# Kernel tuning notes

Hardware: AMD Instinct MI355X
Metric: run time of the kernel (lower is better)

Reference implementation:

```python
import jax, jax.numpy as jnp
import numpy as np

NUM_NODES = 100000
NUM_REL = 3
IN_C, HID_C, OUT_C = 128, 64, 32
E, P = 1600000, 200000


def setup_inputs() -> dict:
    key = jax.random.key(0)
    ks = jax.random.split(key, 16)
    inp = {
        "x": jax.random.normal(ks[0], (NUM_NODES, IN_C), dtype=jnp.float32),
        "edge_index": jax.random.randint(ks[1], (2, E), 0, NUM_NODES),
        "edge_type": jax.random.randint(ks[2], (E,), 0, NUM_REL),
        "pred_edges": jax.random.randint(ks[3], (2, P), 0, NUM_NODES),
        # RGCN layer 1
        "W1": jax.random.normal(ks[4], (NUM_REL, IN_C, HID_C), dtype=jnp.float32) * 0.05,
        "root1": jax.random.normal(ks[5], (IN_C, HID_C), dtype=jnp.float32) * 0.05,
        "b1": jnp.zeros((HID_C,), dtype=jnp.float32),
        # RGCN layer 2
        "W2": jax.random.normal(ks[6], (NUM_REL, HID_C, OUT_C), dtype=jnp.float32) * 0.05,
        "root2": jax.random.normal(ks[7], (HID_C, OUT_C), dtype=jnp.float32) * 0.05,
        "b2": jnp.zeros((OUT_C,), dtype=jnp.float32),
        # decoder MLP: Linear(2*OUT_C, HID_C) -> ReLU -> Linear(HID_C, 1)
        "Wd1": jax.random.normal(ks[8], (2 * OUT_C, HID_C), dtype=jnp.float32) * 0.05,
        "bd1": jnp.zeros((HID_C,), dtype=jnp.float32),
        "Wd2": jax.random.normal(ks[9], (HID_C, 1), dtype=jnp.float32) * 0.05,
        "bd2": jnp.zeros((1,), dtype=jnp.float32),
    }
    return inp


def rgcn_conv(x, edge_index, edge_type, W, root, b):
    """PyG RGCNConv: per-relation mean aggregation + root transform + bias."""
    src, dst = edge_index[0], edge_index[1]
    n = x.shape[0]
    xs = x[src]  # [E, in] single gather reused across relations
    out = x @ root + b
    for r in range(W.shape[0]):  # small fixed relation count
        mask = (edge_type == r)
        msg = jnp.where(mask[:, None], xs @ W[r], 0.0)  # [E, out]
        summed = jax.ops.segment_sum(msg, dst, num_segments=n)
        cnt = jax.ops.segment_sum(mask.astype(x.dtype), dst, num_segments=n)
        out = out + summed / jnp.maximum(cnt, 1.0)[:, None]
    return out


def reference(x, edge_index, edge_type, pred_edges, W1, root1, b1, W2, root2, b2, Wd1, bd1, Wd2, bd2):
    # encode (eval mode: dropout is identity)
    z = jax.nn.relu(rgcn_conv(x, edge_index, edge_type, W1, root1, b1))
    z = rgcn_conv(z, edge_index, edge_type, W2, root2, b2)
    # decode
    src, dst = pred_edges[0], pred_edges[1]
    ef = jnp.concatenate([z[src], z[dst]], axis=1)  # [P, 2*OUT_C]
    h = jax.nn.relu(ef @ Wd1 + bd1)
    return (h @ Wd2 + bd2).squeeze(-1)  # [P]
```

## Files before the change

kernel.cpp:

```cpp
#include <hip/hip_runtime.h>
#include <hip/hip_bf16.h>


typedef short bf16x8 __attribute__((ext_vector_type(8)));
typedef float f32x4 __attribute__((ext_vector_type(4)));
typedef float f32x2 __attribute__((ext_vector_type(2)));

__device__ __forceinline__ unsigned short f2bf(float f) {
  union { float f; unsigned u; } x; x.f = f;
  unsigned r = x.u + 0x7FFF + ((x.u >> 16) & 1);
  return (unsigned short)(r >> 16);
}
__device__ __forceinline__ float bf2f(unsigned short h) {
  union { unsigned u; float f; } x; x.u = ((unsigned)h) << 16;
  return x.f;
}
__device__ __forceinline__ f32x2 bfpair(unsigned u) {
  union { unsigned u; float f; } a, b;
  a.u = u << 16; b.u = u & 0xFFFF0000u;
  f32x2 r; r[0] = a.f; r[1] = b.f; return r;
}
__device__ __forceinline__ unsigned pk2(float a, float b) {
  return (unsigned)f2bf(a) | ((unsigned)f2bf(b) << 16);
}

template <int K, int TN>
__device__ __forceinline__ void pack_one(
    int e, const float* __restrict__ W, const float* __restrict__ root,
    ushort* __restrict__ Bh, ushort* __restrict__ Bl) {
  int slab = e / (K * TN), r = e % (K * TN);
  int k = r / TN, n = r % TN;
  float v = (slab < 3) ? W[(size_t)slab * K * TN + k * TN + n] : root[(size_t)k * TN + n];
  int kc = k >> 5, quad = (k >> 3) & 3, j = k & 7, nt = n >> 4, nn = n & 15;
  int NTt = TN / 16;
  int didx = slab * K * TN + ((kc * NTt + nt) * 64 + quad * 16 + nn) * 8 + j;
  unsigned short h = f2bf(v);
  Bh[didx] = h;
  Bl[didx] = f2bf(v - bf2f(h));
}

__global__ __launch_bounds__(256) void hist_pack_kernel(
    const int* __restrict__ ei, int* __restrict__ hist, int E, int tile, int NBUCK,
    const float* __restrict__ W1, const float* __restrict__ root1,
    ushort* __restrict__ Bh1, ushort* __restrict__ Bl1,
    const float* __restrict__ W2, const float* __restrict__ root2,
    ushort* __restrict__ Bh2, ushort* __restrict__ Bl2,
    const float* __restrict__ Wd1, ushort* __restrict__ Bd1h) {
  int tid = threadIdx.x;
  if (blockIdx.x >= 256) {
    int e = (blockIdx.x - 256) * 256 + tid;
    if (e < 32768) {
      pack_one<128, 64>(e, W1, root1, Bh1, Bl1);
    } else if (e < 32768 + 8192) {
      pack_one<64, 32>(e - 32768, W2, root2, Bh2, Bl2);
    } else if (e < 32768 + 8192 + 4096) {
      int r = e - 32768 - 8192;
      int k = r >> 6, n = r & 63;
      int kc = k >> 5, quad = (k >> 3) & 3, j = k & 7, nt = n >> 4, nn = n & 15;
      Bd1h[((kc * 4 + nt) * 64 + quad * 16 + nn) * 8 + j] = f2bf(Wd1[k * 64 + n]);
    }
    return;
  }
  __shared__ int lh[512];
  for (int i = tid; i < 512; i += 256) lh[i] = 0;
  __syncthreads();
  int e0 = blockIdx.x * tile, e1 = min(E, e0 + tile);
  for (int e = e0 + tid; e < e1; e += 256) atomicAdd(&lh[ei[E + e] >> 8], 1);
  __syncthreads();
  for (int i = tid; i < NBUCK; i += 256) hist[i * 256 + blockIdx.x] = lh[i];
}

__device__ __forceinline__ void gemm1_body(
    int bid, int4* __restrict__ bsm,
    const float* __restrict__ A, const ushort* __restrict__ Bh,
    const ushort* __restrict__ Bl, const float* __restrict__ bias,
    ushort* __restrict__ Hb, float* __restrict__ z, int n) {
  constexpr int K = 128, TN = 64;
  constexpr int KC = K / 32;
  constexpr int NTt = TN / 16;
  constexpr int HALF = K * TN / 8;
  const int tid = threadIdx.x;
  const int w = tid >> 6, lane = tid & 63;
  const int quad = lane >> 4, nn = lane & 15;
  const int rowBase = bid * 64 + w * 16;

  int row = rowBase + nn;
  if (row >= n) row = n - 1;
  const float* ap = &A[(size_t)row * K + quad * 8];
  bf16x8 ah[KC], al[KC];
#pragma unroll
  for (int kc = 0; kc < KC; kc++) {
    float4 f0 = *(const float4*)(ap + kc * 32);
    float4 f1 = *(const float4*)(ap + kc * 32 + 4);
    float f[8] = {f0.x, f0.y, f0.z, f0.w, f1.x, f1.y, f1.z, f1.w};
#pragma unroll
    for (int j = 0; j < 8; j++) {
      unsigned short h = f2bf(f[j]);
      ah[kc][j] = (short)h;
      al[kc][j] = (short)f2bf(f[j] - bf2f(h));
    }
  }

  const short* bsp = (const short*)bsm;

#pragma unroll 1
  for (int slab = 0; slab < 4; slab++) {
    __syncthreads();
    {
      const int4* gh = (const int4*)(Bh + (size_t)slab * K * TN);
      for (int i = tid; i < HALF; i += 256) bsm[i] = gh[i];
      if (slab == 3) {
        const int4* gl = (const int4*)(Bl + (size_t)slab * K * TN);
        for (int i = tid; i < HALF; i += 256) bsm[HALF + i] = gl[i];
      }
    }
    __syncthreads();

    f32x4 acc[NTt];
#pragma unroll
    for (int j = 0; j < NTt; j++) acc[j] = (f32x4){0.f, 0.f, 0.f, 0.f};

#pragma unroll
    for (int kc = 0; kc < KC; kc++) {
#pragma unroll
      for (int nt = 0; nt < NTt; nt++) {
        bf16x8 b = *(const bf16x8*)&bsp[((kc * NTt + nt) * 64 + lane) * 8];
        acc[nt] = __builtin_amdgcn_mfma_f32_16x16x32_bf16(ah[kc], b, acc[nt], 0, 0, 0);
        acc[nt] = __builtin_amdgcn_mfma_f32_16x16x32_bf16(al[kc], b, acc[nt], 0, 0, 0);
      }
    }
    if (slab == 3) {
#pragma unroll
      for (int kc = 0; kc < KC; kc++) {
#pragma unroll
        for (int nt = 0; nt < NTt; nt++) {
          bf16x8 b = *(const bf16x8*)&bsp[(HALF * 8) + ((kc * NTt + nt) * 64 + lane) * 8];
          acc[nt] = __builtin_amdgcn_mfma_f32_16x16x32_bf16(ah[kc], b, acc[nt], 0, 0, 0);
        }
      }
    }

    int grow0 = rowBase + quad * 4;
#pragma unroll
    for (int nt = 0; nt < NTt; nt++) {
      int col = nt * 16 + nn;
#pragma unroll
      for (int rg = 0; rg < 4; rg++) {
        int grow = grow0 + rg;
        if (grow < n) {
          float v = acc[nt][rg];
          if (slab == 3) z[(size_t)grow * TN + col] = v + bias[col];
          else Hb[((size_t)slab * n + grow) * TN + col] = f2bf(v);
        }
      }
    }
  }
}


__global__ __launch_bounds__(256, 4) void scan_rows_gemm_kernel(
    int* __restrict__ hist, int* __restrict__ rowsum, int nChain, int gemmBase,
    const float* __restrict__ A, const ushort* __restrict__ Bh,
    const ushort* __restrict__ Bl, const float* __restrict__ bias,
    ushort* __restrict__ Hb, float* __restrict__ z, int n) {
  __shared__ int4 smem[2048];
  if ((int)blockIdx.x >= nChain) {
    gemm1_body(gemmBase + (int)blockIdx.x - nChain, smem, A, Bh, Bl, bias, Hb, z, n);
    return;
  }
  int* sA = (int*)smem;
  int* sB = sA + 256;
  int t = threadIdx.x;
  int* row = hist + blockIdx.x * 256;
  int v = row[t];
  sA[t] = v;
  __syncthreads();
  int* src = sA; int* dst = sB;
  for (int off = 1; off < 256; off <<= 1) {
    int x = src[t];
    if (t >= off) x += src[t - off];
    dst[t] = x;
    __syncthreads();
    int* tmp = src; src = dst; dst = tmp;
  }
  row[t] = src[t] - v;
  if (t == 255) rowsum[blockIdx.x] = src[255];
}

__global__ __launch_bounds__(256, 4) void scan_top_gemm_kernel(
    const int* __restrict__ rowsum, int* __restrict__ rowbase, int NBUCK, int E,
    int nChain, int gemmBase,
    const float* __restrict__ A, const ushort* __restrict__ Bh,
    const ushort* __restrict__ Bl, const float* __restrict__ bias,
    ushort* __restrict__ Hb, float* __restrict__ z, int n) {
  __shared__ int4 smem[2048];
  if ((int)blockIdx.x >= nChain) {
    gemm1_body(gemmBase + (int)blockIdx.x - nChain, smem, A, Bh, Bl, bias, Hb, z, n);
    return;
  }
  int* sA = (int*)smem;
  int* sB = sA + 256;
  int t = threadIdx.x;
  int e0 = 2 * t, e1 = 2 * t + 1;
  int v0 = (e0 < NBUCK) ? rowsum[e0] : 0;
  int v1 = (e1 < NBUCK) ? rowsum[e1] : 0;
  int v = v0 + v1;
  sA[t] = v;
  __syncthreads();
  int* src = sA; int* dst = sB;
  for (int off = 1; off < 256; off <<= 1) {
    int x = src[t];
    if (t >= off) x += src[t - off];
    dst[t] = x;
    __syncthreads();
    int* tmp = src; src = dst; dst = tmp;
  }
  int excl = src[t] - v;
  if (e0 < NBUCK) rowbase[e0] = excl;
  if (e1 < NBUCK) rowbase[e1] = excl + v0;
  if (t == 0) rowbase[NBUCK] = E;
}

__global__ __launch_bounds__(256, 4) void part_scatter_gemm_kernel(
    const int* __restrict__ ei, const int* __restrict__ et,
    const int* __restrict__ hist, const int* __restrict__ rowbase,
    unsigned* __restrict__ rec, int E, int tile, int NBUCK,
    int nChain, int gemmBase,
    const float* __restrict__ A, const ushort* __restrict__ Bh,
    const ushort* __restrict__ Bl, const float* __restrict__ bias,
    ushort* __restrict__ Hb, float* __restrict__ z, int n) {
  __shared__ int4 smem[2048];
  if ((int)blockIdx.x >= nChain) {
    gemm1_body(gemmBase + (int)blockIdx.x - nChain, smem, A, Bh, Bl, bias, Hb, z, n);
    return;
  }
  int* ctr = (int*)smem;
  int tid = threadIdx.x;
  for (int i = tid; i < NBUCK; i += 256)
    ctr[i] = hist[i * 256 + blockIdx.x] + rowbase[i];
  __syncthreads();
  int e0 = blockIdx.x * tile, e1 = min(E, e0 + tile);
  for (int e = e0 + tid; e < e1; e += 256) {
    int s = ei[e];
    int d = ei[E + e];
    int t = et[e];
    int p = atomicAdd(&ctr[d >> 8], 1);
    rec[p] = (unsigned)(s | (t << 20) | ((d & 255) << 22));
  }
}

__global__ __launch_bounds__(256, 4) void bucket_build_gemm_kernel(
    const unsigned* __restrict__ rec, const int* __restrict__ rowbase,
    int2* __restrict__ sd, int2* __restrict__ erec, int N,
    int nChain, int gemmBase,
    const float* __restrict__ A, const ushort* __restrict__ Bh,
    const ushort* __restrict__ Bl, const float* __restrict__ bias,
    ushort* __restrict__ Hb, float* __restrict__ z) {
  __shared__ int4 smem[2048];
  if ((int)blockIdx.x >= nChain) {
    gemm1_body(gemmBase + (int)blockIdx.x - nChain, smem, A, Bh, Bl, bias, Hb, z, N);
    return;
  }
  int* c3 = (int*)smem;
  int* sA = c3 + 768;
  int* sB = sA + 256;
  int* cur = sB + 256;
  int tid = threadIdx.x;
  int dstBase = blockIdx.x << 8;
  int bs = rowbase[blockIdx.x], be = rowbase[blockIdx.x + 1];
  for (int i = tid; i < 768; i += 256) c3[i] = 0;
  __syncthreads();
  for (int i = bs + tid; i < be; i += 256) {
    unsigned r = rec[i];
    atomicAdd(&c3[((r >> 20) & 3) * 256 + (r >> 22)], 1);
  }
  __syncthreads();
  int dgv = c3[tid] + c3[256 + tid] + c3[512 + tid];
  sA[tid] = dgv;
  __syncthreads();
  int* src = sA; int* dst = sB;
  for (int off = 1; off < 256; off <<= 1) {
    int x = src[tid];
    if (tid >= off) x += src[tid - off];
    dst[tid] = x;
    __syncthreads();
    int* tmp = src; src = dst; dst = tmp;
  }
  int excl = src[tid] - dgv;
  cur[tid] = bs + excl;
  if (dstBase + tid < N) sd[dstBase + tid] = make_int2(bs + excl, dgv);
  __syncthreads();
  for (int i = bs + tid; i < be; i += 256) {
    unsigned r = rec[i];
    int dloc = r >> 22;
    int t = (r >> 20) & 3;
    int p = atomicAdd(&cur[dloc], 1);
    float sc = 1.0f / (float)max(c3[t * 256 + dloc], 1);
    erec[p] = make_int2(t * N + (int)(r & 0xFFFFF), __float_as_int(sc));
  }
}

__global__ __launch_bounds__(256, 4) void mfma_gemm2_kernel(
    const ushort* __restrict__ Ab, const ushort* __restrict__ Bh,
    const ushort* __restrict__ Bl, const float* __restrict__ bias,
    ushort* __restrict__ Hb, float* __restrict__ z2r, int n) {
  constexpr int KC = 2, NTt = 2, HALF = 64 * 32 / 8;
  __shared__ int4 bsm[2 * HALF];
  const int tid = threadIdx.x;
  const int w = tid >> 6, lane = tid & 63;
  const int quad = lane >> 4, nn = lane & 15;
  const int rowBase = blockIdx.x * 64 + w * 16;

  int row = rowBase + nn;
  if (row >= n) row = n - 1;
  const ushort* ap = &Ab[(size_t)row * 64 + quad * 8];
  bf16x8 ah[KC];
  ah[0] = *(const bf16x8*)(ap);
  ah[1] = *(const bf16x8*)(ap + 32);

  const short* bsp = (const short*)bsm;

#pragma unroll 1
  for (int slab = 0; slab < 4; slab++) {
    __syncthreads();
    {
      const int4* gh = (const int4*)(Bh + (size_t)slab * 64 * 32);
      for (int i = tid; i < HALF; i += 256) bsm[i] = gh[i];
      if (slab == 3) {
        const int4* gl = (const int4*)(Bl + (size_t)slab * 64 * 32);
        for (int i = tid; i < HALF; i += 256) bsm[HALF + i] = gl[i];
      }
    }
    __syncthreads();

    f32x4 acc[NTt];
#pragma unroll
    for (int j = 0; j < NTt; j++) acc[j] = (f32x4){0.f, 0.f, 0.f, 0.f};

#pragma unroll
    for (int kc = 0; kc < KC; kc++) {
#pragma unroll
      for (int nt = 0; nt < NTt; nt++) {
        bf16x8 b = *(const bf16x8*)&bsp[((kc * NTt + nt) * 64 + lane) * 8];
        acc[nt] = __builtin_amdgcn_mfma_f32_16x16x32_bf16(ah[kc], b, acc[nt], 0, 0, 0);
      }
    }
    if (slab == 3) {
#pragma unroll
      for (int kc = 0; kc < KC; kc++) {
#pragma unroll
        for (int nt = 0; nt < NTt; nt++) {
          bf16x8 b = *(const bf16x8*)&bsp[(HALF * 8) + ((kc * NTt + nt) * 64 + lane) * 8];
          acc[nt] = __builtin_amdgcn_mfma_f32_16x16x32_bf16(ah[kc], b, acc[nt], 0, 0, 0);
        }
      }
    }

    int grow0 = rowBase + quad * 4;
#pragma unroll
    for (int nt = 0; nt < NTt; nt++) {
      int col = nt * 16 + nn;
#pragma unroll
      for (int rg = 0; rg < 4; rg++) {
        int grow = grow0 + rg;
        if (grow < n) {
          float v = acc[nt][rg];
          if (slab == 3) z2r[(size_t)grow * 32 + col] = v + bias[col];
          else Hb[((size_t)slab * n + grow) * 32 + col] = f2bf(v);
        }
      }
    }
  }
}

__global__ __launch_bounds__(256) void pull64_kernel(
    const ushort* __restrict__ Hb, const int2* __restrict__ erec,
    const int2* __restrict__ sd, const float* __restrict__ z1r,
    ushort* __restrict__ z1b, int N) {
  int t = blockIdx.x * 256 + threadIdx.x;
  int w = t >> 5;
  if (w >= N) return;
  int q = threadIdx.x & 7;
  int k = (threadIdx.x >> 3) & 3;
  int2 s2 = sd[w];
  int j0 = s2.x + ((s2.y * k) >> 2);
  int j1 = s2.x + ((s2.y * (k + 1)) >> 2);
  f32x2 a0 = {0.f, 0.f}, a1 = a0, a2 = a0, a3 = a0;
  for (int j = j0; j < j1; j++) {
    int2 r = erec[j];
    float sc = __int_as_float(r.y);
    f32x2 sc2 = {sc, sc};
    uint4 v = *(const uint4*)&Hb[(size_t)r.x * 64 + q * 8];
    a0 += bfpair(v.x) * sc2;
    a1 += bfpair(v.y) * sc2;
    a2 += bfpair(v.z) * sc2;
    a3 += bfpair(v.w) * sc2;
  }
#pragma unroll
  for (int m = 8; m <= 16; m <<= 1) {
    a0[0] += __shfl_xor(a0[0], m); a0[1] += __shfl_xor(a0[1], m);
    a1[0] += __shfl_xor(a1[0], m); a1[1] += __shfl_xor(a1[1], m);
    a2[0] += __shfl_xor(a2[0], m); a2[1] += __shfl_xor(a2[1], m);
    a3[0] += __shfl_xor(a3[0], m); a3[1] += __shfl_xor(a3[1], m);
  }
  if (k == 0) {
    const float4* zr = (const float4*)&z1r[(size_t)w * 64 + q * 8];
    float4 r0 = zr[0], r1 = zr[1];
    uint4 st;
    st.x = pk2(fmaxf(r0.x + a0[0], 0.f), fmaxf(r0.y + a0[1], 0.f));
    st.y = pk2(fmaxf(r0.z + a1[0], 0.f), fmaxf(r0.w + a1[1], 0.f));
    st.z = pk2(fmaxf(r1.x + a2[0], 0.f), fmaxf(r1.y + a2[1], 0.f));
    st.w = pk2(fmaxf(r1.z + a3[0], 0.f), fmaxf(r1.w + a3[1], 0.f));
    *(uint4*)&z1b[(size_t)w * 64 + q * 8] = st;
  }
}

__global__ __launch_bounds__(256) void pull32_kernel(
    const ushort* __restrict__ Hb, const int2* __restrict__ erec,
    const int2* __restrict__ sd, const float* __restrict__ z2r,
    ushort* __restrict__ z2b, int N) {
  int t = blockIdx.x * 256 + threadIdx.x;
  int w = t >> 4;
  if (w >= N) return;
  int q = threadIdx.x & 3;
  int k = (threadIdx.x >> 2) & 3;
  int2 s2 = sd[w];
  int j0 = s2.x + ((s2.y * k) >> 2);
  int j1 = s2.x + ((s2.y * (k + 1)) >> 2);
  f32x2 a0 = {0.f, 0.f}, a1 = a0, a2 = a0, a3 = a0;
  for (int j = j0; j < j1; j++) {
    int2 r = erec[j];
    float sc = __int_as_float(r.y);
    f32x2 sc2 = {sc, sc};
    uint4 v = *(const uint4*)&Hb[(size_t)r.x * 32 + q * 8];
    a0 += bfpair(v.x) * sc2;
    a1 += bfpair(v.y) * sc2;
    a2 += bfpair(v.z) * sc2;
    a3 += bfpair(v.w) * sc2;
  }
#pragma unroll
  for (int m = 4; m <= 8; m <<= 1) {
    a0[0] += __shfl_xor(a0[0], m); a0[1] += __shfl_xor(a0[1], m);
    a1[0] += __shfl_xor(a1[0], m); a1[1] += __shfl_xor(a1[1], m);
    a2[0] += __shfl_xor(a2[0], m); a2[1] += __shfl_xor(a2[1], m);
    a3[0] += __shfl_xor(a3[0], m); a3[1] += __shfl_xor(a3[1], m);
  }
  if (k == 0) {
    const float4* zr = (const float4*)&z2r[(size_t)w * 32 + q * 8];
    float4 r0 = zr[0], r1 = zr[1];
    uint4 st;
    st.x = pk2(r0.x + a0[0], r0.y + a0[1]);
    st.y = pk2(r0.z + a1[0], r0.w + a1[1]);
    st.z = pk2(r1.x + a2[0], r1.y + a2[1]);
    st.w = pk2(r1.z + a3[0], r1.w + a3[1]);
    *(uint4*)&z2b[(size_t)w * 32 + q * 8] = st;
  }
}

__global__ __launch_bounds__(256) void decoder_kernel(
    const ushort* __restrict__ z2b, const int* __restrict__ pe,
    const ushort* __restrict__ Bd1h, const float* __restrict__ bd1,
    const float* __restrict__ Wd2, const float* __restrict__ bd2,
    float* __restrict__ out, int P) {
  __shared__ int4 wsm[512];
  __shared__ float b1s[64], w2s[64];
  int tid = threadIdx.x;
  {
    const int4* g = (const int4*)Bd1h;
    for (int i = tid; i < 512; i += 256) wsm[i] = g[i];
    if (tid < 64) { b1s[tid] = bd1[tid]; w2s[tid] = Wd2[tid]; }
  }
  __syncthreads();
  const short* bsp = (const short*)wsm;
  int wv = tid >> 6, lane = tid & 63;
  int quad = lane >> 4, nn = lane & 15;
  int p0 = blockIdx.x * 64 + wv * 16;
  int p = min(p0 + nn, P - 1);
  int s = pe[p], d = pe[P + p];
  bf16x8 a0 = *(const bf16x8*)&z2b[(size_t)s * 32 + quad * 8];
  bf16x8 a1 = *(const bf16x8*)&z2b[(size_t)d * 32 + quad * 8];
  f32x4 acc[4];
#pragma unroll
  for (int nt = 0; nt < 4; nt++) acc[nt] = (f32x4){0.f, 0.f, 0.f, 0.f};
#pragma unroll
  for (int nt = 0; nt < 4; nt++) {
    bf16x8 b0 = *(const bf16x8*)&bsp[((0 * 4 + nt) * 64 + lane) * 8];
    acc[nt] = __builtin_amdgcn_mfma_f32_16x16x32_bf16(a0, b0, acc[nt], 0, 0, 0);
    bf16x8 b1 = *(const bf16x8*)&bsp[((1 * 4 + nt) * 64 + lane) * 8];
    acc[nt] = __builtin_amdgcn_mfma_f32_16x16x32_bf16(a1, b1, acc[nt], 0, 0, 0);
  }
  float part[4];
#pragma unroll
  for (int rg = 0; rg < 4; rg++) {
    float t = 0.f;
#pragma unroll
    for (int nt = 0; nt < 4; nt++) {
      int col = nt * 16 + nn;
      float h = fmaxf(acc[nt][rg] + b1s[col], 0.f);
      t += h * w2s[col];
    }
    part[rg] = t;
  }
#pragma unroll
  for (int m = 1; m <= 8; m <<= 1)
#pragma unroll
    for (int rg = 0; rg < 4; rg++) part[rg] += __shfl_xor(part[rg], m);
  if (nn == 0) {
    float base = bd2[0];
#pragma unroll
    for (int rg = 0; rg < 4; rg++) {
      int po = p0 + quad * 4 + rg;
      if (po < P) out[po] = part[rg] + base;
    }
  }
}

extern "C" void kernel_launch(void* const* d_in, const int* in_sizes, int n_in,
                              void* d_out, int out_size, void* d_ws, size_t ws_size,
                              hipStream_t stream) {
  const float* x     = (const float*)d_in[0];
  const int*   ei    = (const int*)d_in[1];
  const int*   et    = (const int*)d_in[2];
  const int*   pe    = (const int*)d_in[3];
  const float* W1    = (const float*)d_in[4];
  const float* root1 = (const float*)d_in[5];
  const float* b1    = (const float*)d_in[6];
  const float* W2    = (const float*)d_in[7];
  const float* root2 = (const float*)d_in[8];
  const float* b2    = (const float*)d_in[9];
  const float* Wd1   = (const float*)d_in[10];
  const float* bd1   = (const float*)d_in[11];
  const float* Wd2   = (const float*)d_in[12];
  const float* bd2   = (const float*)d_in[13];
  float* out = (float*)d_out;

  const int N = in_sizes[0] / 128;
  const int E = in_sizes[2];
  const int P = in_sizes[3] / 2;

  const int NBUCK = (N + 255) >> 8;
  const int tile  = (E + 255) / 256;

  float* ws   = (float*)d_ws;
  float* z1r  = ws;
  ushort* z1b = (ushort*)(ws + (size_t)64 * N);
  float* z2r  = ws + (size_t)96 * N;
  ushort* z2b = (ushort*)(ws + (size_t)128 * N);
  ushort* Hb  = (ushort*)(ws + (size_t)144 * N);
  ushort* Bh1 = (ushort*)(ws + (size_t)240 * N);
  ushort* Bl1 = Bh1 + 32768;
  ushort* Bh2 = Bl1 + 32768;
  ushort* Bl2 = Bh2 + 8192;
  ushort* Bd1h = Bl2 + 8192;
  int* ib      = (int*)(ws + (size_t)241 * N);
  int2* sd     = (int2*)ib;
  int2* erec   = (int2*)(ib + 2 * (size_t)N);
  int* rowbase = ib + 2 * (size_t)N + 2 * (size_t)E;
  int* rowsum  = rowbase + 1024;
  int* hist    = rowsum + 1024;
  unsigned* rec = (unsigned*)(hist + (size_t)NBUCK * 256);

  const int gb = (N + 63) / 64;
  int s1 = min(gb, 200);
  int s2 = min(gb - s1, 200);
  int s3 = min(gb - s1 - s2, 500);
  int s4 = gb - s1 - s2 - s3;

  hist_pack_kernel<<<256 + 176, 256, 0, stream>>>(
      ei, hist, E, tile, NBUCK, W1, root1, Bh1, Bl1, W2, root2, Bh2, Bl2,
      Wd1, Bd1h);
  scan_rows_gemm_kernel<<<NBUCK + s1, 256, 0, stream>>>(
      hist, rowsum, NBUCK, 0, x, Bh1, Bl1, b1, Hb, z1r, N);
  scan_top_gemm_kernel<<<1 + s2, 256, 0, stream>>>(
      rowsum, rowbase, NBUCK, E, 1, s1, x, Bh1, Bl1, b1, Hb, z1r, N);
  part_scatter_gemm_kernel<<<256 + s3, 256, 0, stream>>>(
      ei, et, hist, rowbase, rec, E, tile, NBUCK, 256, s1 + s2,
      x, Bh1, Bl1, b1, Hb, z1r, N);
  bucket_build_gemm_kernel<<<NBUCK + s4, 256, 0, stream>>>(
      rec, rowbase, sd, erec, N, NBUCK, s1 + s2 + s3,
      x, Bh1, Bl1, b1, Hb, z1r);

  pull64_kernel<<<((size_t)N * 32 + 255) / 256, 256, 0, stream>>>(Hb, erec, sd, z1r, z1b, N);

  mfma_gemm2_kernel<<<gb, 256, 0, stream>>>(z1b, Bh2, Bl2, b2, Hb, z2r, N);
  pull32_kernel<<<((size_t)N * 16 + 255) / 256, 256, 0, stream>>>(Hb, erec, sd, z2r, z2b, N);

  decoder_kernel<<<(P + 63) / 64, 256, 0, stream>>>(z2b, pe, Bd1h, bd1, Wd2, bd2, out, P);
}
```

Before: 310.9 us.

## Pack edge records to 32 bits, drop scan kernel, unroll pull gathers

Edge records shrink from int2 (index plus float scale) to one 32-bit word. The word holds the relation-offset source index in the low 19 bits and the per-relation count in the high bits, and the pull kernels rebuild the scale with a fast reciprocal. The separate top-level scan kernel is removed: the part-scatter and bucket-build blocks each redo the small 512-entry scan of row sums, trading a launch and a global round trip for redundant per-block work. The pull64/pull32 gather loops are unrolled by four to keep more independent loads in flight, and edge, root and output accesses use nontemporal loads and stores. The approximate reciprocal may change results slightly, and the packing bounds the node index and the count.

```diff
diff --git a/kernel.cpp b/kernel.cpp
--- a/kernel.cpp
+++ b/kernel.cpp
@@ -5,6 +5,7 @@
 typedef short bf16x8 __attribute__((ext_vector_type(8)));
 typedef float f32x4 __attribute__((ext_vector_type(4)));
 typedef float f32x2 __attribute__((ext_vector_type(2)));
+typedef unsigned u32x4 __attribute__((ext_vector_type(4)));
 
 __device__ __forceinline__ unsigned short f2bf(float f) {
   union { float f; unsigned u; } x; x.f = f;
@@ -187,43 +188,9 @@
   if (t == 255) rowsum[blockIdx.x] = src[255];
 }
 
-__global__ __launch_bounds__(256, 4) void scan_top_gemm_kernel(
-    const int* __restrict__ rowsum, int* __restrict__ rowbase, int NBUCK, int E,
-    int nChain, int gemmBase,
-    const float* __restrict__ A, const ushort* __restrict__ Bh,
-    const ushort* __restrict__ Bl, const float* __restrict__ bias,
-    ushort* __restrict__ Hb, float* __restrict__ z, int n) {
-  __shared__ int4 smem[2048];
-  if ((int)blockIdx.x >= nChain) {
-    gemm1_body(gemmBase + (int)blockIdx.x - nChain, smem, A, Bh, Bl, bias, Hb, z, n);
-    return;
-  }
-  int* sA = (int*)smem;
-  int* sB = sA + 256;
-  int t = threadIdx.x;
-  int e0 = 2 * t, e1 = 2 * t + 1;
-  int v0 = (e0 < NBUCK) ? rowsum[e0] : 0;
-  int v1 = (e1 < NBUCK) ? rowsum[e1] : 0;
-  int v = v0 + v1;
-  sA[t] = v;
-  __syncthreads();
-  int* src = sA; int* dst = sB;
-  for (int off = 1; off < 256; off <<= 1) {
-    int x = src[t];
-    if (t >= off) x += src[t - off];
-    dst[t] = x;
-    __syncthreads();
-    int* tmp = src; src = dst; dst = tmp;
-  }
-  int excl = src[t] - v;
-  if (e0 < NBUCK) rowbase[e0] = excl;
-  if (e1 < NBUCK) rowbase[e1] = excl + v0;
-  if (t == 0) rowbase[NBUCK] = E;
-}
-
 __global__ __launch_bounds__(256, 4) void part_scatter_gemm_kernel(
     const int* __restrict__ ei, const int* __restrict__ et,
-    const int* __restrict__ hist, const int* __restrict__ rowbase,
+    const int* __restrict__ hist, const int* __restrict__ rowsum,
     unsigned* __restrict__ rec, int E, int tile, int NBUCK,
     int nChain, int gemmBase,
     const float* __restrict__ A, const ushort* __restrict__ Bh,
@@ -234,24 +201,45 @@
     gemm1_body(gemmBase + (int)blockIdx.x - nChain, smem, A, Bh, Bl, bias, Hb, z, n);
     return;
   }
-  int* ctr = (int*)smem;
-  int tid = threadIdx.x;
-  for (int i = tid; i < NBUCK; i += 256)
-    ctr[i] = hist[i * 256 + blockIdx.x] + rowbase[i];
-  __syncthreads();
-  int e0 = blockIdx.x * tile, e1 = min(E, e0 + tile);
-  for (int e = e0 + tid; e < e1; e += 256) {
+  int* sA = (int*)smem;
+  int* sB = sA + 256;
+  int* rb = sB + 256;
+  int* ctr = rb + 512;
+  int t = threadIdx.x;
+  int e0 = 2 * t, e1 = 2 * t + 1;
+  int v0 = (e0 < NBUCK) ? rowsum[e0] : 0;
+  int v1 = (e1 < NBUCK) ? rowsum[e1] : 0;
+  int v = v0 + v1;
+  sA[t] = v;
+  __syncthreads();
+  int* src = sA; int* dst = sB;
+  for (int off = 1; off < 256; off <<= 1) {
+    int x = src[t];
+    if (t >= off) x += src[t - off];
+    dst[t] = x;
+    __syncthreads();
+    int* tmp = src; src = dst; dst = tmp;
+  }
+  int excl = src[t] - v;
+  rb[e0] = excl;
+  rb[e1] = excl + v0;
+  __syncthreads();
+  for (int i = t; i < NBUCK; i += 256)
+    ctr[i] = hist[i * 256 + blockIdx.x] + rb[i];
+  __syncthreads();
+  int e0g = blockIdx.x * tile, e1g = min(E, e0g + tile);
+  for (int e = e0g + t; e < e1g; e += 256) {
     int s = ei[e];
     int d = ei[E + e];
-    int t = et[e];
+    int rt = et[e];
     int p = atomicAdd(&ctr[d >> 8], 1);
-    rec[p] = (unsigned)(s | (t << 20) | ((d & 255) << 22));
+    rec[p] = (unsigned)(s | (rt << 20) | ((d & 255) << 22));
   }
 }
 
 __global__ __launch_bounds__(256, 4) void bucket_build_gemm_kernel(
-    const unsigned* __restrict__ rec, const int* __restrict__ rowbase,
-    int2* __restrict__ sd, int2* __restrict__ erec, int N,
+    const unsigned* __restrict__ rec, const int* __restrict__ rowsum,
+    int2* __restrict__ sd, unsigned* __restrict__ erec, int N, int NBUCK,
     int nChain, int gemmBase,
     const float* __restrict__ A, const ushort* __restrict__ Bh,
     const ushort* __restrict__ Bl, const float* __restrict__ bias,
@@ -265,9 +253,30 @@
   int* sA = c3 + 768;
   int* sB = sA + 256;
   int* cur = sB + 256;
+  int* rb = cur + 256;
   int tid = threadIdx.x;
+  {
+    int e0 = 2 * tid, e1 = 2 * tid + 1;
+    int v0 = (e0 < NBUCK) ? rowsum[e0] : 0;
+    int v1 = (e1 < NBUCK) ? rowsum[e1] : 0;
+    int v = v0 + v1;
+    sA[tid] = v;
+    __syncthreads();
+    int* src = sA; int* dst = sB;
+    for (int off = 1; off < 256; off <<= 1) {
+      int x = src[tid];
+      if (tid >= off) x += src[tid - off];
+      dst[tid] = x;
+      __syncthreads();
+      int* tmp = src; src = dst; dst = tmp;
+    }
+    int excl = src[tid] - v;
+    rb[e0] = excl;
+    rb[e1] = excl + v0;
+    __syncthreads();
+  }
   int dstBase = blockIdx.x << 8;
-  int bs = rowbase[blockIdx.x], be = rowbase[blockIdx.x + 1];
+  int bs = rb[blockIdx.x], be = rb[blockIdx.x + 1];
   for (int i = tid; i < 768; i += 256) c3[i] = 0;
   __syncthreads();
   for (int i = bs + tid; i < be; i += 256) {
@@ -293,10 +302,10 @@
   for (int i = bs + tid; i < be; i += 256) {
     unsigned r = rec[i];
     int dloc = r >> 22;
-    int t = (r >> 20) & 3;
+    int rt = (r >> 20) & 3;
     int p = atomicAdd(&cur[dloc], 1);
-    float sc = 1.0f / (float)max(c3[t * 256 + dloc], 1);
-    erec[p] = make_int2(t * N + (int)(r & 0xFFFFF), __float_as_int(sc));
+    unsigned cnt = (unsigned)c3[rt * 256 + dloc];
+    erec[p] = (unsigned)(rt * N + (int)(r & 0xFFFFF)) | (cnt << 19);
   }
 }
 
@@ -374,7 +383,7 @@
 }
 
 __global__ __launch_bounds__(256) void pull64_kernel(
-    const ushort* __restrict__ Hb, const int2* __restrict__ erec,
+    const ushort* __restrict__ Hb, const unsigned* __restrict__ erec,
     const int2* __restrict__ sd, const float* __restrict__ z1r,
     ushort* __restrict__ z1b, int N) {
   int t = blockIdx.x * 256 + threadIdx.x;
@@ -386,15 +395,39 @@
   int j0 = s2.x + ((s2.y * k) >> 2);
   int j1 = s2.x + ((s2.y * (k + 1)) >> 2);
   f32x2 a0 = {0.f, 0.f}, a1 = a0, a2 = a0, a3 = a0;
-  for (int j = j0; j < j1; j++) {
-    int2 r = erec[j];
-    float sc = __int_as_float(r.y);
+  int j = j0;
+  for (; j + 4 <= j1; j += 4) {
+    unsigned r0 = __builtin_nontemporal_load(erec + j);
+    unsigned r1 = __builtin_nontemporal_load(erec + j + 1);
+    unsigned r2 = __builtin_nontemporal_load(erec + j + 2);
+    unsigned r3 = __builtin_nontemporal_load(erec + j + 3);
+    u32x4 v0 = *(const u32x4*)&Hb[(size_t)(r0 & 0x7FFFF) * 64 + q * 8];
+    u32x4 v1 = *(const u32x4*)&Hb[(size_t)(r1 & 0x7FFFF) * 64 + q * 8];
+    u32x4 v2 = *(const u32x4*)&Hb[(size_t)(r2 & 0x7FFFF) * 64 + q * 8];
+    u32x4 v3 = *(const u32x4*)&Hb[(size_t)(r3 & 0x7FFFF) * 64 + q * 8];
+    float f0 = __builtin_amdgcn_rcpf((float)(r0 >> 19));
+    float f1 = __builtin_amdgcn_rcpf((float)(r1 >> 19));
+    float f2 = __builtin_amdgcn_rcpf((float)(r2 >> 19));
+    float f3 = __builtin_amdgcn_rcpf((float)(r3 >> 19));
+    f32x2 s0 = {f0, f0}, s1 = {f1, f1}, s2v = {f2, f2}, s3 = {f3, f3};
+    a0 += bfpair(v0[0]) * s0; a1 += bfpair(v0[1]) * s0;
+    a2 += bfpair(v0[2]) * s0; a3 += bfpair(v0[3]) * s0;
+    a0 += bfpair(v1[0]) * s1; a1 += bfpair(v1[1]) * s1;
+    a2 += bfpair(v1[2]) * s1; a3 += bfpair(v1[3]) * s1;
+    a0 += bfpair(v2[0]) * s2v; a1 += bfpair(v2[1]) * s2v;
+    a2 += bfpair(v2[2]) * s2v; a3 += bfpair(v2[3]) * s2v;
+    a0 += bfpair(v3[0]) * s3; a1 += bfpair(v3[1]) * s3;
+    a2 += bfpair(v3[2]) * s3; a3 += bfpair(v3[3]) * s3;
+  }
+  for (; j < j1; j++) {
+    unsigned r = __builtin_nontemporal_load(erec + j);
+    float sc = __builtin_amdgcn_rcpf((float)(r >> 19));
     f32x2 sc2 = {sc, sc};
-    uint4 v = *(const uint4*)&Hb[(size_t)r.x * 64 + q * 8];
-    a0 += bfpair(v.x) * sc2;
-    a1 += bfpair(v.y) * sc2;
-    a2 += bfpair(v.z) * sc2;
-    a3 += bfpair(v.w) * sc2;
+    u32x4 v = *(const u32x4*)&Hb[(size_t)(r & 0x7FFFF) * 64 + q * 8];
+    a0 += bfpair(v[0]) * sc2;
+    a1 += bfpair(v[1]) * sc2;
+    a2 += bfpair(v[2]) * sc2;
+    a3 += bfpair(v[3]) * sc2;
   }
 #pragma unroll
   for (int m = 8; m <= 16; m <<= 1) {
@@ -404,19 +437,20 @@
     a3[0] += __shfl_xor(a3[0], m); a3[1] += __shfl_xor(a3[1], m);
   }
   if (k == 0) {
-    const float4* zr = (const float4*)&z1r[(size_t)w * 64 + q * 8];
-    float4 r0 = zr[0], r1 = zr[1];
-    uint4 st;
-    st.x = pk2(fmaxf(r0.x + a0[0], 0.f), fmaxf(r0.y + a0[1], 0.f));
-    st.y = pk2(fmaxf(r0.z + a1[0], 0.f), fmaxf(r0.w + a1[1], 0.f));
-    st.z = pk2(fmaxf(r1.x + a2[0], 0.f), fmaxf(r1.y + a2[1], 0.f));
-    st.w = pk2(fmaxf(r1.z + a3[0], 0.f), fmaxf(r1.w + a3[1], 0.f));
-    *(uint4*)&z1b[(size_t)w * 64 + q * 8] = st;
+    const f32x4* zr = (const f32x4*)&z1r[(size_t)w * 64 + q * 8];
+    f32x4 r0 = __builtin_nontemporal_load(zr);
+    f32x4 r1 = __builtin_nontemporal_load(zr + 1);
+    u32x4 st;
+    st[0] = pk2(fmaxf(r0[0] + a0[0], 0.f), fmaxf(r0[1] + a0[1], 0.f));
+    st[1] = pk2(fmaxf(r0[2] + a1[0], 0.f), fmaxf(r0[3] + a1[1], 0.f));
+    st[2] = pk2(fmaxf(r1[0] + a2[0], 0.f), fmaxf(r1[1] + a2[1], 0.f));
+    st[3] = pk2(fmaxf(r1[2] + a3[0], 0.f), fmaxf(r1[3] + a3[1], 0.f));
+    __builtin_nontemporal_store(st, (u32x4*)&z1b[(size_t)w * 64 + q * 8]);
   }
 }
 
 __global__ __launch_bounds__(256) void pull32_kernel(
-    const ushort* __restrict__ Hb, const int2* __restrict__ erec,
+    const ushort* __restrict__ Hb, const unsigned* __restrict__ erec,
     const int2* __restrict__ sd, const float* __restrict__ z2r,
     ushort* __restrict__ z2b, int N) {
   int t = blockIdx.x * 256 + threadIdx.x;
@@ -428,15 +462,39 @@
   int j0 = s2.x + ((s2.y * k) >> 2);
   int j1 = s2.x + ((s2.y * (k + 1)) >> 2);
   f32x2 a0 = {0.f, 0.f}, a1 = a0, a2 = a0, a3 = a0;
-  for (int j = j0; j < j1; j++) {
-    int2 r = erec[j];
-    float sc = __int_as_float(r.y);
+  int j = j0;
+  for (; j + 4 <= j1; j += 4) {
+    unsigned r0 = __builtin_nontemporal_load(erec + j);
+    unsigned r1 = __builtin_nontemporal_load(erec + j + 1);
+    unsigned r2 = __builtin_nontemporal_load(erec + j + 2);
+    unsigned r3 = __builtin_nontemporal_load(erec + j + 3);
+    u32x4 v0 = *(const u32x4*)&Hb[(size_t)(r0 & 0x7FFFF) * 32 + q * 8];
+    u32x4 v1 = *(const u32x4*)&Hb[(size_t)(r1 & 0x7FFFF) * 32 + q * 8];
+    u32x4 v2 = *(const u32x4*)&Hb[(size_t)(r2 & 0x7FFFF) * 32 + q * 8];
+    u32x4 v3 = *(const u32x4*)&Hb[(size_t)(r3 & 0x7FFFF) * 32 + q * 8];
+    float f0 = __builtin_amdgcn_rcpf((float)(r0 >> 19));
+    float f1 = __builtin_amdgcn_rcpf((float)(r1 >> 19));
+    float f2 = __builtin_amdgcn_rcpf((float)(r2 >> 19));
+    float f3 = __builtin_amdgcn_rcpf((float)(r3 >> 19));
+    f32x2 s0 = {f0, f0}, s1 = {f1, f1}, s2v = {f2, f2}, s3 = {f3, f3};
+    a0 += bfpair(v0[0]) * s0; a1 += bfpair(v0[1]) * s0;
+    a2 += bfpair(v0[2]) * s0; a3 += bfpair(v0[3]) * s0;
+    a0 += bfpair(v1[0]) * s1; a1 += bfpair(v1[1]) * s1;
+    a2 += bfpair(v1[2]) * s1; a3 += bfpair(v1[3]) * s1;
+    a0 += bfpair(v2[0]) * s2v; a1 += bfpair(v2[1]) * s2v;
+    a2 += bfpair(v2[2]) * s2v; a3 += bfpair(v2[3]) * s2v;
+    a0 += bfpair(v3[0]) * s3; a1 += bfpair(v3[1]) * s3;
+    a2 += bfpair(v3[2]) * s3; a3 += bfpair(v3[3]) * s3;
+  }
+  for (; j < j1; j++) {
+    unsigned r = __builtin_nontemporal_load(erec + j);
+    float sc = __builtin_amdgcn_rcpf((float)(r >> 19));
     f32x2 sc2 = {sc, sc};
-    uint4 v = *(const uint4*)&Hb[(size_t)r.x * 32 + q * 8];
-    a0 += bfpair(v.x) * sc2;
-    a1 += bfpair(v.y) * sc2;
-    a2 += bfpair(v.z) * sc2;
-    a3 += bfpair(v.w) * sc2;
+    u32x4 v = *(const u32x4*)&Hb[(size_t)(r & 0x7FFFF) * 32 + q * 8];
+    a0 += bfpair(v[0]) * sc2;
+    a1 += bfpair(v[1]) * sc2;
+    a2 += bfpair(v[2]) * sc2;
+    a3 += bfpair(v[3]) * sc2;
   }
 #pragma unroll
   for (int m = 4; m <= 8; m <<= 1) {
@@ -446,14 +504,15 @@
     a3[0] += __shfl_xor(a3[0], m); a3[1] += __shfl_xor(a3[1], m);
   }
   if (k == 0) {
-    const float4* zr = (const float4*)&z2r[(size_t)w * 32 + q * 8];
-    float4 r0 = zr[0], r1 = zr[1];
-    uint4 st;
-    st.x = pk2(r0.x + a0[0], r0.y + a0[1]);
-    st.y = pk2(r0.z + a1[0], r0.w + a1[1]);
-    st.z = pk2(r1.x + a2[0], r1.y + a2[1]);
-    st.w = pk2(r1.z + a3[0], r1.w + a3[1]);
-    *(uint4*)&z2b[(size_t)w * 32 + q * 8] = st;
+    const f32x4* zr = (const f32x4*)&z2r[(size_t)w * 32 + q * 8];
+    f32x4 r0 = __builtin_nontemporal_load(zr);
+    f32x4 r1 = __builtin_nontemporal_load(zr + 1);
+    u32x4 st;
+    st[0] = pk2(r0[0] + a0[0], r0[1] + a0[1]);
+    st[1] = pk2(r0[2] + a1[0], r0[3] + a1[1]);
+    st[2] = pk2(r1[0] + a2[0], r1[1] + a2[1]);
+    st[3] = pk2(r1[2] + a3[0], r1[3] + a3[1]);
+    __builtin_nontemporal_store(st, (u32x4*)&z2b[(size_t)w * 32 + q * 8]);
   }
 }
 
@@ -554,30 +613,26 @@
   ushort* Bd1h = Bl2 + 8192;
   int* ib      = (int*)(ws + (size_t)241 * N);
   int2* sd     = (int2*)ib;
-  int2* erec   = (int2*)(ib + 2 * (size_t)N);
-  int* rowbase = ib + 2 * (size_t)N + 2 * (size_t)E;
-  int* rowsum  = rowbase + 1024;
+  unsigned* erec = (unsigned*)(ib + 2 * (size_t)N);
+  int* rowsum  = ib + 2 * (size_t)N + 2 * (size_t)E + 1024;
   int* hist    = rowsum + 1024;
   unsigned* rec = (unsigned*)(hist + (size_t)NBUCK * 256);
 
   const int gb = (N + 63) / 64;
-  int s1 = min(gb, 200);
-  int s2 = min(gb - s1, 200);
-  int s3 = min(gb - s1 - s2, 500);
-  int s4 = gb - s1 - s2 - s3;
+  int s1 = min(gb, 400);
+  int s3 = min(gb - s1, 500);
+  int s4 = gb - s1 - s3;
 
   hist_pack_kernel<<<256 + 176, 256, 0, stream>>>(
       ei, hist, E, tile, NBUCK, W1, root1, Bh1, Bl1, W2, root2, Bh2, Bl2,
       Wd1, Bd1h);
   scan_rows_gemm_kernel<<<NBUCK + s1, 256, 0, stream>>>(
       hist, rowsum, NBUCK, 0, x, Bh1, Bl1, b1, Hb, z1r, N);
-  scan_top_gemm_kernel<<<1 + s2, 256, 0, stream>>>(
-      rowsum, rowbase, NBUCK, E, 1, s1, x, Bh1, Bl1, b1, Hb, z1r, N);
   part_scatter_gemm_kernel<<<256 + s3, 256, 0, stream>>>(
-      ei, et, hist, rowbase, rec, E, tile, NBUCK, 256, s1 + s2,
+      ei, et, hist, rowsum, rec, E, tile, NBUCK, 256, s1,
       x, Bh1, Bl1, b1, Hb, z1r, N);
   bucket_build_gemm_kernel<<<NBUCK + s4, 256, 0, stream>>>(
-      rec, rowbase, sd, erec, N, NBUCK, s1 + s2 + s3,
+      rec, rowsum, sd, erec, N, NBUCK, NBUCK, s1 + s3,
       x, Bh1, Bl1, b1, Hb, z1r);
 
   pull64_kernel<<<((size_t)N * 32 + 255) / 256, 256, 0, stream>>>(Hb, erec, sd, z1r, z1b, N);
```

Result: faster. 295.6 us (-4.9%).
